# Optimization experiments

Hardware: AMD Instinct MI355X
Metric: run time of the kernel (lower is better)

## Reference

```python
import jax, jax.numpy as jnp
import numpy as np
from jax.ops import segment_sum


def gcn_conv(x, edge_index, W, b):
    """PyG GCNConv: add self-loops, symmetric D^-1/2 (A+I) D^-1/2 normalization,
    then aggregate normalized messages at target nodes. edge_weight=None -> ones."""
    N = x.shape[0]
    loops = jnp.arange(N, dtype=edge_index.dtype)
    row = jnp.concatenate([edge_index[0], loops])  # source nodes
    col = jnp.concatenate([edge_index[1], loops])  # target nodes
    w = jnp.ones(row.shape[0], dtype=x.dtype)
    deg = segment_sum(w, col, num_segments=N)
    dinv = jnp.where(deg > 0, jax.lax.rsqrt(deg), 0.0)
    norm = dinv[row] * dinv[col]                    # [E+N]
    xw = x @ W                                      # dense transform [N, out]
    msg = xw[row] * norm[:, None]                   # gather + scale [E+N, out]
    out = segment_sum(msg, col, num_segments=N)     # scatter-add at targets
    return out + b


def setup_inputs() -> dict:
    key = jax.random.key(0)
    k1, k2, k3, k4 = jax.random.split(key, 4)
    N, E, nhid, nfeat = 50000, 800000, 256, 128
    x = jax.random.normal(k1, (N, nhid), dtype=jnp.float32)
    edge_index = jax.random.randint(k2, (2, E), 0, N, dtype=jnp.int64)
    W1 = jax.random.normal(k3, (nhid, nhid), dtype=jnp.float32) * (1.0 / np.sqrt(nhid))
    b1 = jnp.zeros((nhid,), dtype=jnp.float32)
    W2 = jax.random.normal(k4, (nhid, nfeat), dtype=jnp.float32) * (1.0 / np.sqrt(nhid))
    b2 = jnp.zeros((nfeat,), dtype=jnp.float32)
    return {"x": x, "edge_index": edge_index, "W1": W1, "b1": b1, "W2": W2, "b2": b2}


def reference(x, edge_index, W1, b1, W2, b2):
    h = jax.nn.relu(gcn_conv(x, edge_index, W1, b1))
    # dropout is identity in eval mode (deterministic reference)
    return gcn_conv(h, edge_index, W2, b2)
```

## Files before the change

kernel.cpp:

```cpp
#include <hip/hip_runtime.h>
#include <math.h>


typedef _Float16 h8 __attribute__((ext_vector_type(8)));
typedef float    f32x4 __attribute__((ext_vector_type(4)));

#define CAP 64

__global__ void k_init(int* __restrict__ deg, int* __restrict__ govf, int N,
                       const float* __restrict__ W1, const float* __restrict__ W2,
                       _Float16* __restrict__ wt1, _Float16* __restrict__ wt2,
                       int K, int n1, int n2, int zb)
{
    if ((int)blockIdx.x < zb) {
        int i = blockIdx.x * blockDim.x + threadIdx.x;
        if (i < N) deg[i] = 0;
        if (blockIdx.x == 0 && threadIdx.x == 0) *govf = 0;
    } else {
        int i = (blockIdx.x - zb) * blockDim.x + threadIdx.x;
        int c1 = K * n1;
        if (i < c1) {
            int k = i / n1, n = i % n1;
            wt1[(long)n * K + k] = (_Float16)W1[i];
        } else if (i < c1 + K * n2) {
            int j = i - c1;
            int k = j / n2, n = j % n2;
            wt2[(long)n * K + k] = (_Float16)W2[j];
        }
    }
}

template<bool A32>
__device__ __forceinline__ void gemm_body(
    const float* __restrict__ X32, const _Float16* __restrict__ X16,
    const _Float16* __restrict__ Wt, _Float16* __restrict__ Y,
    int M, int K, int NC, int bx, int by)
{
    __shared__ _Float16 As[128][40];
    __shared__ _Float16 Bs[128][40];

    const int bn = bx * 128;
    const int bm = by * 128;
    const int tid = threadIdx.x;
    const int w = tid >> 6, l = tid & 63;
    const int wm = (w >> 1) * 64, wn = (w & 1) * 64;
    const int lr = l & 15, lg = l >> 4;

    const int arow = tid >> 2, acol = (tid & 3) * 8;
    const int xrow = tid >> 1, xcol = (tid & 1) * 16;

    f32x4 acc[4][4];
    #pragma unroll
    for (int i = 0; i < 4; i++)
        #pragma unroll
        for (int j = 0; j < 4; j++)
            acc[i][j] = (f32x4){0.f, 0.f, 0.f, 0.f};

    float4 pf0, pf1, pf2, pf3;
    h8 pa0, pa1;
    h8 pb0, pb1;

    auto loadA = [&](int k0) {
        if (A32) {
            int gm0 = bm + arow;      if (gm0 >= M) gm0 = M - 1;
            int gm1 = bm + 64 + arow; if (gm1 >= M) gm1 = M - 1;
            pf0 = *reinterpret_cast<const float4*>(&X32[(long)gm0 * K + k0 + acol]);
            pf1 = *reinterpret_cast<const float4*>(&X32[(long)gm0 * K + k0 + acol + 4]);
            pf2 = *reinterpret_cast<const float4*>(&X32[(long)gm1 * K + k0 + acol]);
            pf3 = *reinterpret_cast<const float4*>(&X32[(long)gm1 * K + k0 + acol + 4]);
        } else {
            int gm = bm + xrow; if (gm >= M) gm = M - 1;
            pa0 = *reinterpret_cast<const h8*>(&X16[(long)gm * K + k0 + xcol]);
            pa1 = *reinterpret_cast<const h8*>(&X16[(long)gm * K + k0 + xcol + 8]);
        }
    };
    auto loadB = [&](int k0) {
        pb0 = *reinterpret_cast<const h8*>(&Wt[(long)(bn + xrow) * K + k0 + xcol]);
        pb1 = *reinterpret_cast<const h8*>(&Wt[(long)(bn + xrow) * K + k0 + xcol + 8]);
    };

    loadA(0); loadB(0);
    for (int k0 = 0; k0 < K; k0 += 32) {
        if (A32) {
            h8 h0, h1;
            h0[0] = (_Float16)pf0.x; h0[1] = (_Float16)pf0.y;
            h0[2] = (_Float16)pf0.z; h0[3] = (_Float16)pf0.w;
            h0[4] = (_Float16)pf1.x; h0[5] = (_Float16)pf1.y;
            h0[6] = (_Float16)pf1.z; h0[7] = (_Float16)pf1.w;
            h1[0] = (_Float16)pf2.x; h1[1] = (_Float16)pf2.y;
            h1[2] = (_Float16)pf2.z; h1[3] = (_Float16)pf2.w;
            h1[4] = (_Float16)pf3.x; h1[5] = (_Float16)pf3.y;
            h1[6] = (_Float16)pf3.z; h1[7] = (_Float16)pf3.w;
            *reinterpret_cast<h8*>(&As[arow][acol]) = h0;
            *reinterpret_cast<h8*>(&As[64 + arow][acol]) = h1;
        } else {
            *reinterpret_cast<h8*>(&As[xrow][xcol]) = pa0;
            *reinterpret_cast<h8*>(&As[xrow][xcol + 8]) = pa1;
        }
        *reinterpret_cast<h8*>(&Bs[xrow][xcol]) = pb0;
        *reinterpret_cast<h8*>(&Bs[xrow][xcol + 8]) = pb1;
        __syncthreads();

        if (k0 + 32 < K) { loadA(k0 + 32); loadB(k0 + 32); }

        h8 a[4], b[4];
        #pragma unroll
        for (int i = 0; i < 4; i++)
            a[i] = *reinterpret_cast<const h8*>(&As[wm + i * 16 + lr][lg * 8]);
        #pragma unroll
        for (int j = 0; j < 4; j++)
            b[j] = *reinterpret_cast<const h8*>(&Bs[wn + j * 16 + lr][lg * 8]);
        #pragma unroll
        for (int i = 0; i < 4; i++)
            #pragma unroll
            for (int j = 0; j < 4; j++)
                acc[i][j] = __builtin_amdgcn_mfma_f32_16x16x32_f16(
                    a[i], b[j], acc[i][j], 0, 0, 0);
        __syncthreads();
    }

    #pragma unroll
    for (int i = 0; i < 4; i++) {
        #pragma unroll
        for (int r = 0; r < 4; r++) {
            int gm = bm + wm + i * 16 + lg * 4 + r;
            if (gm < M) {
                #pragma unroll
                for (int j = 0; j < 4; j++)
                    Y[(long)gm * NC + bn + wn + j * 16 + lr] =
                        (_Float16)acc[i][j][r];
            }
        }
    }
}

__global__ __launch_bounds__(256) void k_count_gemm(
    const int* __restrict__ col, int E, int* __restrict__ deg, int* __restrict__ rank,
    int ncb,
    const float* __restrict__ X32, const _Float16* __restrict__ Wt,
    _Float16* __restrict__ Y, int M, int K, int NC, int gx)
{
    if ((int)blockIdx.x < ncb) {
        int i = blockIdx.x * blockDim.x + threadIdx.x;
        int s = ncb * blockDim.x;
        for (int e = i; e < E; e += s) rank[e] = atomicAdd(&deg[col[e]], 1);
        return;
    }
    int gb = blockIdx.x - ncb;
    gemm_body<true>(X32, nullptr, Wt, Y, M, K, NC, gb % gx, gb / gx);
}

__global__ __launch_bounds__(256) void k_fill_dinv(
    const int* __restrict__ row, const int* __restrict__ col,
    const int* __restrict__ rank, int E,
    const int* __restrict__ deg, float* __restrict__ dinv, int N,
    int* __restrict__ srcidx, int2* __restrict__ ovf, int* __restrict__ govf,
    int zb)
{
    if ((int)blockIdx.x < zb) {
        int i = blockIdx.x * blockDim.x + threadIdx.x;
        if (i < N) dinv[i] = rsqrtf(1.f + (float)deg[i]);
        return;
    }
    int g = (blockIdx.x - zb) * blockDim.x + threadIdx.x;
    int nthreads = (gridDim.x - zb) * blockDim.x;
    if ((E & 3) == 0) {
        int G4 = E >> 2;
        for (int q = g; q < G4; q += nthreads) {
            int e = q << 2;
            int4 c4 = *reinterpret_cast<const int4*>(&col[e]);
            int4 r4 = *reinterpret_cast<const int4*>(&row[e]);
            int4 k4 = *reinterpret_cast<const int4*>(&rank[e]);
            if (k4.x < CAP) srcidx[c4.x * CAP + k4.x] = r4.x;
            else { int o = atomicAdd(govf, 1); ovf[o] = make_int2(r4.x, c4.x); }
            if (k4.y < CAP) srcidx[c4.y * CAP + k4.y] = r4.y;
            else { int o = atomicAdd(govf, 1); ovf[o] = make_int2(r4.y, c4.y); }
            if (k4.z < CAP) srcidx[c4.z * CAP + k4.z] = r4.z;
            else { int o = atomicAdd(govf, 1); ovf[o] = make_int2(r4.z, c4.z); }
            if (k4.w < CAP) srcidx[c4.w * CAP + k4.w] = r4.w;
            else { int o = atomicAdd(govf, 1); ovf[o] = make_int2(r4.w, c4.w); }
        }
    } else {
        for (int e = g; e < E; e += nthreads) {
            int c = col[e], r = row[e], k = rank[e];
            if (k < CAP) srcidx[c * CAP + k] = r;
            else { int o = atomicAdd(govf, 1); ovf[o] = make_int2(r, c); }
        }
    }
}

__global__ __launch_bounds__(256) void k_gemm16(
    const _Float16* __restrict__ X16, const _Float16* __restrict__ Wt,
    _Float16* __restrict__ Y, int M, int K, int NC)
{
    gemm_body<false>(nullptr, X16, Wt, Y, M, K, NC, blockIdx.x, blockIdx.y);
}

template<int LPR, bool F16OUT, bool RELU>
__global__ __launch_bounds__(256) void k_agg(
    const int* __restrict__ deg, const float* __restrict__ dinv,
    const int* __restrict__ srcidx,
    const int2* __restrict__ ovf, const int* __restrict__ govf,
    const _Float16* __restrict__ Y, const float* __restrict__ bias,
    int N, int FT, int fo,
    float* __restrict__ out32, _Float16* __restrict__ out16)
{
    const int G = 64 / LPR;
    int node = blockIdx.x * 4 + (threadIdx.x >> 6);
    if (node >= N) return;
    int lane = threadIdx.x & 63;
    int sub = lane / LPR;
    int fl  = lane % LPR;
    const int fcol = fo + fl * 8;

    float dc = dinv[node];
    int cnt = min(deg[node], CAP);
    const int beg = node * CAP;

    float acc[8];
    if (sub == 0) {
        h8 v = *reinterpret_cast<const h8*>(&Y[(long)node * FT + fcol]);
        #pragma unroll
        for (int j = 0; j < 8; j++) acc[j] = dc * (float)v[j];
    } else {
        #pragma unroll
        for (int j = 0; j < 8; j++) acc[j] = 0.f;
    }

    int i = sub;
    int full = cnt / (4 * G);
    for (int t = 0; t < full; t++) {
        int r0 = srcidx[beg + i];
        int r1 = srcidx[beg + i + G];
        int r2 = srcidx[beg + i + 2 * G];
        int r3 = srcidx[beg + i + 3 * G];
        float d0 = dinv[r0], d1 = dinv[r1], d2 = dinv[r2], d3 = dinv[r3];
        h8 v0 = *reinterpret_cast<const h8*>(&Y[(long)r0 * FT + fcol]);
        h8 v1 = *reinterpret_cast<const h8*>(&Y[(long)r1 * FT + fcol]);
        h8 v2 = *reinterpret_cast<const h8*>(&Y[(long)r2 * FT + fcol]);
        h8 v3 = *reinterpret_cast<const h8*>(&Y[(long)r3 * FT + fcol]);
        #pragma unroll
        for (int j = 0; j < 8; j++)
            acc[j] += (d0 * (float)v0[j] + d1 * (float)v1[j]) +
                      (d2 * (float)v2[j] + d3 * (float)v3[j]);
        i += 4 * G;
    }
    for (; i < cnt; i += G) {
        int r = srcidx[beg + i];
        float d = dinv[r];
        h8 v = *reinterpret_cast<const h8*>(&Y[(long)r * FT + fcol]);
        #pragma unroll
        for (int j = 0; j < 8; j++) acc[j] += d * (float)v[j];
    }
    {
        int no = *govf;
        for (int t = sub; t < no; t += G) {
            int2 pr = ovf[t];
            if (pr.y == node) {
                float d = dinv[pr.x];
                h8 v = *reinterpret_cast<const h8*>(&Y[(long)pr.x * FT + fcol]);
                #pragma unroll
                for (int j = 0; j < 8; j++) acc[j] += d * (float)v[j];
            }
        }
    }

    #pragma unroll
    for (int m = LPR; m < 64; m <<= 1)
        #pragma unroll
        for (int j = 0; j < 8; j++)
            acc[j] += __shfl_xor(acc[j], m, 64);

    const float4* b4 = reinterpret_cast<const float4*>(&bias[fcol]);
    float4 blo = b4[0], bhi = b4[1];
    float r8[8];
    r8[0] = fmaf(dc, acc[0], blo.x); r8[1] = fmaf(dc, acc[1], blo.y);
    r8[2] = fmaf(dc, acc[2], blo.z); r8[3] = fmaf(dc, acc[3], blo.w);
    r8[4] = fmaf(dc, acc[4], bhi.x); r8[5] = fmaf(dc, acc[5], bhi.y);
    r8[6] = fmaf(dc, acc[6], bhi.z); r8[7] = fmaf(dc, acc[7], bhi.w);
    if (RELU) {
        #pragma unroll
        for (int j = 0; j < 8; j++) r8[j] = fmaxf(r8[j], 0.f);
    }

    long base = (long)node * FT + fcol;
    if (F16OUT) {
        if (sub == 0) {
            h8 o;
            #pragma unroll
            for (int j = 0; j < 8; j++) o[j] = (_Float16)r8[j];
            *reinterpret_cast<h8*>(&out16[base]) = o;
        }
    } else {
        if (sub == 0) {
            *reinterpret_cast<float4*>(&out32[base]) =
                make_float4(r8[0], r8[1], r8[2], r8[3]);
        } else if (sub == 1) {
            *reinterpret_cast<float4*>(&out32[base + 4]) =
                make_float4(r8[4], r8[5], r8[6], r8[7]);
        }
    }
}

extern "C" void kernel_launch(void* const* d_in, const int* in_sizes, int n_in,
                              void* d_out, int out_size, void* d_ws, size_t ws_size,
                              hipStream_t stream)
{
    const float* x   = (const float*)d_in[0];
    const int*   ei  = (const int*)d_in[1];
    const float* W1  = (const float*)d_in[2];
    const float* b1  = (const float*)d_in[3];
    const float* W2  = (const float*)d_in[4];
    const float* b2  = (const float*)d_in[5];

    const int nhid  = in_sizes[3];
    const int nfeat = in_sizes[5];
    const int N     = in_sizes[0] / nhid;
    const int E     = in_sizes[1] / 2;

    const int* row = ei;
    const int* col = ei + E;

    size_t cur = 0;
    auto alloc = [&](size_t bytes) {
        void* p = (char*)d_ws + cur;
        cur += (bytes + 255) & ~(size_t)255;
        return p;
    };
    float*     dinv   = (float*)alloc((size_t)N * 4);
    int*       deg_i  = (int*)alloc((size_t)N * 4);
    int*       rank   = (int*)alloc((size_t)E * 4);
    int*       srcidx = (int*)alloc((size_t)N * CAP * 4);
    int2*      ovf    = (int2*)alloc((size_t)E * 8);
    int*       govf   = (int*)alloc(256);
    _Float16*  wt1    = (_Float16*)alloc((size_t)nhid * nhid * 2);
    _Float16*  wt2    = (_Float16*)alloc((size_t)nhid * nfeat * 2);
    _Float16*  y16    = (_Float16*)alloc((size_t)N * nhid * 2);
    _Float16*  h16    = (_Float16*)alloc((size_t)N * nhid * 2);
    _Float16*  y2     = (_Float16*)alloc((size_t)N * nfeat * 2);
    float*     out    = (float*)d_out;
    (void)ws_size; (void)n_in; (void)out_size;

    const int T = 256;
    const int zb = (N + T - 1) / T;

    {
        int pb = (nhid * (nhid + nfeat) + T - 1) / T;
        k_init<<<zb + pb, T, 0, stream>>>(deg_i, govf, N, W1, W2, wt1, wt2,
                                          nhid, nhid, nfeat, zb);
    }

    {
        const int ncb = 256;
        int gx = nhid / 128;
        int gy = (N + 127) / 128;
        k_count_gemm<<<ncb + gx * gy, T, 0, stream>>>(
            col, E, deg_i, rank, ncb, x, wt1, y16, N, nhid, nhid, gx);
    }

    k_fill_dinv<<<zb + 1024, T, 0, stream>>>(
        row, col, rank, E, deg_i, dinv, N, srcidx, ovf, govf, zb);

    k_agg<16, true, true><<<(N + 3) / 4, T, 0, stream>>>(
        deg_i, dinv, srcidx, ovf, govf, y16, b1, N, nhid, 0, nullptr, h16);
    k_agg<16, true, true><<<(N + 3) / 4, T, 0, stream>>>(
        deg_i, dinv, srcidx, ovf, govf, y16, b1, N, nhid, 128, nullptr, h16);

    {
        dim3 grid(nfeat / 128, (N + 127) / 128);
        k_gemm16<<<grid, T, 0, stream>>>(h16, wt2, y2, N, nhid, nfeat);
    }
    k_agg<16, false, false><<<(N + 3) / 4, T, 0, stream>>>(
        deg_i, dinv, srcidx, ovf, govf, y2, b2, N, nfeat, 0, out, nullptr);
}
```

Baseline: 180.5 us.

## Split first GEMM column tiles across count and fill kernels for overlap

The first-layer GEMM tiles are now split in half by output column block: one half runs alongside the degree-count atomics, the other half alongside the dinv and bucket-fill work in the following kernel. The count grid also grows from 256 to 512 blocks. The aim is to balance each launch so the memory-bound edge work hides behind compute-bound GEMM blocks, rather than putting all GEMM work into the first launch. The risk is that the GEMM halves now contend with the different edge phases for bandwidth and CUs.

```diff
diff --git a/kernel.cpp b/kernel.cpp
--- a/kernel.cpp
+++ b/kernel.cpp
@@ -138,7 +138,7 @@
     const int* __restrict__ col, int E, int* __restrict__ deg, int* __restrict__ rank,
     int ncb,
     const float* __restrict__ X32, const _Float16* __restrict__ Wt,
-    _Float16* __restrict__ Y, int M, int K, int NC, int gx)
+    _Float16* __restrict__ Y, int M, int K, int NC, int gxA, int bx0)
 {
     if ((int)blockIdx.x < ncb) {
         int i = blockIdx.x * blockDim.x + threadIdx.x;
@@ -147,46 +147,53 @@
         return;
     }
     int gb = blockIdx.x - ncb;
-    gemm_body<true>(X32, nullptr, Wt, Y, M, K, NC, gb % gx, gb / gx);
-}
-
-__global__ __launch_bounds__(256) void k_fill_dinv(
+    gemm_body<true>(X32, nullptr, Wt, Y, M, K, NC, bx0 + gb % gxA, gb / gxA);
+}
+
+__global__ __launch_bounds__(256) void k_fill_gemm(
     const int* __restrict__ row, const int* __restrict__ col,
     const int* __restrict__ rank, int E,
     const int* __restrict__ deg, float* __restrict__ dinv, int N,
     int* __restrict__ srcidx, int2* __restrict__ ovf, int* __restrict__ govf,
-    int zb)
+    int zb, int nfb,
+    const float* __restrict__ X32, const _Float16* __restrict__ Wt,
+    _Float16* __restrict__ Y, int M, int K, int NC, int gxB, int bx0)
 {
     if ((int)blockIdx.x < zb) {
         int i = blockIdx.x * blockDim.x + threadIdx.x;
         if (i < N) dinv[i] = rsqrtf(1.f + (float)deg[i]);
         return;
     }
-    int g = (blockIdx.x - zb) * blockDim.x + threadIdx.x;
-    int nthreads = (gridDim.x - zb) * blockDim.x;
-    if ((E & 3) == 0) {
-        int G4 = E >> 2;
-        for (int q = g; q < G4; q += nthreads) {
-            int e = q << 2;
-            int4 c4 = *reinterpret_cast<const int4*>(&col[e]);
-            int4 r4 = *reinterpret_cast<const int4*>(&row[e]);
-            int4 k4 = *reinterpret_cast<const int4*>(&rank[e]);
-            if (k4.x < CAP) srcidx[c4.x * CAP + k4.x] = r4.x;
-            else { int o = atomicAdd(govf, 1); ovf[o] = make_int2(r4.x, c4.x); }
-            if (k4.y < CAP) srcidx[c4.y * CAP + k4.y] = r4.y;
-            else { int o = atomicAdd(govf, 1); ovf[o] = make_int2(r4.y, c4.y); }
-            if (k4.z < CAP) srcidx[c4.z * CAP + k4.z] = r4.z;
-            else { int o = atomicAdd(govf, 1); ovf[o] = make_int2(r4.z, c4.z); }
-            if (k4.w < CAP) srcidx[c4.w * CAP + k4.w] = r4.w;
-            else { int o = atomicAdd(govf, 1); ovf[o] = make_int2(r4.w, c4.w); }
-        }
-    } else {
-        for (int e = g; e < E; e += nthreads) {
-            int c = col[e], r = row[e], k = rank[e];
-            if (k < CAP) srcidx[c * CAP + k] = r;
-            else { int o = atomicAdd(govf, 1); ovf[o] = make_int2(r, c); }
-        }
-    }
+    if ((int)blockIdx.x < zb + nfb) {
+        int g = (blockIdx.x - zb) * blockDim.x + threadIdx.x;
+        int nthreads = nfb * blockDim.x;
+        if ((E & 3) == 0) {
+            int G4 = E >> 2;
+            for (int q = g; q < G4; q += nthreads) {
+                int e = q << 2;
+                int4 c4 = *reinterpret_cast<const int4*>(&col[e]);
+                int4 r4 = *reinterpret_cast<const int4*>(&row[e]);
+                int4 k4 = *reinterpret_cast<const int4*>(&rank[e]);
+                if (k4.x < CAP) srcidx[c4.x * CAP + k4.x] = r4.x;
+                else { int o = atomicAdd(govf, 1); ovf[o] = make_int2(r4.x, c4.x); }
+                if (k4.y < CAP) srcidx[c4.y * CAP + k4.y] = r4.y;
+                else { int o = atomicAdd(govf, 1); ovf[o] = make_int2(r4.y, c4.y); }
+                if (k4.z < CAP) srcidx[c4.z * CAP + k4.z] = r4.z;
+                else { int o = atomicAdd(govf, 1); ovf[o] = make_int2(r4.z, c4.z); }
+                if (k4.w < CAP) srcidx[c4.w * CAP + k4.w] = r4.w;
+                else { int o = atomicAdd(govf, 1); ovf[o] = make_int2(r4.w, c4.w); }
+            }
+        } else {
+            for (int e = g; e < E; e += nthreads) {
+                int c = col[e], r = row[e], k = rank[e];
+                if (k < CAP) srcidx[c * CAP + k] = r;
+                else { int o = atomicAdd(govf, 1); ovf[o] = make_int2(r, c); }
+            }
+        }
+        return;
+    }
+    int gb = blockIdx.x - zb - nfb;
+    gemm_body<true>(X32, nullptr, Wt, Y, M, K, NC, bx0 + gb % gxB, gb / gxB);
 }
 
 __global__ __launch_bounds__(256) void k_gemm16(
@@ -343,6 +350,10 @@
 
     const int T = 256;
     const int zb = (N + T - 1) / T;
+    const int gx = nhid / 128;
+    const int gy = (N + 127) / 128;
+    const int gxA = (gx + 1) / 2;
+    const int gxB = gx - gxA;
 
     {
         int pb = (nhid * (nhid + nfeat) + T - 1) / T;
@@ -351,15 +362,17 @@
     }
 
     {
-        const int ncb = 256;
-        int gx = nhid / 128;
-        int gy = (N + 127) / 128;
-        k_count_gemm<<<ncb + gx * gy, T, 0, stream>>>(
-            col, E, deg_i, rank, ncb, x, wt1, y16, N, nhid, nhid, gx);
-    }
-
-    k_fill_dinv<<<zb + 1024, T, 0, stream>>>(
-        row, col, rank, E, deg_i, dinv, N, srcidx, ovf, govf, zb);
+        const int ncb = 512;
+        k_count_gemm<<<ncb + gxA * gy, T, 0, stream>>>(
+            col, E, deg_i, rank, ncb, x, wt1, y16, N, nhid, nhid, gxA, 0);
+    }
+
+    {
+        const int nfb = 1024;
+        k_fill_gemm<<<zb + nfb + gxB * gy, T, 0, stream>>>(
+            row, col, rank, E, deg_i, dinv, N, srcidx, ovf, govf, zb, nfb,
+            x, wt1, y16, N, nhid, nhid, gxB, gxA);
+    }
 
     k_agg<16, true, true><<<(N + 3) / 4, T, 0, stream>>>(
         deg_i, dinv, srcidx, ovf, govf, y16, b1, N, nhid, 0, nullptr, h16);
```

Measured after the change: 195.3 us. +8.2%, slower.

## Reschedule kernels: memset init, fuse weight prep with count, GEMM with fill

Applied to the files above, without the earlier changes.

Replaces the init kernel with a hipMemsetAsync over the degree counter and overflow counter, which are now allocated next to each other. The fp16 weight transpose moves into the degree-count kernel, which also gets more counting blocks. The first GEMM now runs alongside the dinv/srcidx fill instead of alongside the count. The two feature-half layer-1 aggregation launches merge into one launch that picks the feature offset from the block index. This cuts launch count and rebalances which independent work overlaps, at the cost of a memset node and changed dependencies: the GEMM now waits for the count and weight prep.

```diff
diff --git a/kernel.cpp b/kernel.cpp
--- a/kernel.cpp
+++ b/kernel.cpp
@@ -6,29 +6,6 @@
 typedef float    f32x4 __attribute__((ext_vector_type(4)));
 
 #define CAP 64
-
-__global__ void k_init(int* __restrict__ deg, int* __restrict__ govf, int N,
-                       const float* __restrict__ W1, const float* __restrict__ W2,
-                       _Float16* __restrict__ wt1, _Float16* __restrict__ wt2,
-                       int K, int n1, int n2, int zb)
-{
-    if ((int)blockIdx.x < zb) {
-        int i = blockIdx.x * blockDim.x + threadIdx.x;
-        if (i < N) deg[i] = 0;
-        if (blockIdx.x == 0 && threadIdx.x == 0) *govf = 0;
-    } else {
-        int i = (blockIdx.x - zb) * blockDim.x + threadIdx.x;
-        int c1 = K * n1;
-        if (i < c1) {
-            int k = i / n1, n = i % n1;
-            wt1[(long)n * K + k] = (_Float16)W1[i];
-        } else if (i < c1 + K * n2) {
-            int j = i - c1;
-            int k = j / n2, n = j % n2;
-            wt2[(long)n * K + k] = (_Float16)W2[j];
-        }
-    }
-}
 
 template<bool A32>
 __device__ __forceinline__ void gemm_body(
@@ -134,11 +111,12 @@
     }
 }
 
-__global__ __launch_bounds__(256) void k_count_gemm(
+__global__ __launch_bounds__(256) void k_count_prep(
     const int* __restrict__ col, int E, int* __restrict__ deg, int* __restrict__ rank,
     int ncb,
-    const float* __restrict__ X32, const _Float16* __restrict__ Wt,
-    _Float16* __restrict__ Y, int M, int K, int NC, int gx)
+    const float* __restrict__ W1, const float* __restrict__ W2,
+    _Float16* __restrict__ wt1, _Float16* __restrict__ wt2,
+    int K, int n1, int n2)
 {
     if ((int)blockIdx.x < ncb) {
         int i = blockIdx.x * blockDim.x + threadIdx.x;
@@ -146,24 +124,39 @@
         for (int e = i; e < E; e += s) rank[e] = atomicAdd(&deg[col[e]], 1);
         return;
     }
-    int gb = blockIdx.x - ncb;
-    gemm_body<true>(X32, nullptr, Wt, Y, M, K, NC, gb % gx, gb / gx);
-}
-
-__global__ __launch_bounds__(256) void k_fill_dinv(
+    int i = (blockIdx.x - ncb) * blockDim.x + threadIdx.x;
+    int c1 = K * n1;
+    if (i < c1) {
+        int k = i / n1, n = i % n1;
+        wt1[(long)n * K + k] = (_Float16)W1[i];
+    } else if (i < c1 + K * n2) {
+        int j = i - c1;
+        int k = j / n2, n = j % n2;
+        wt2[(long)n * K + k] = (_Float16)W2[j];
+    }
+}
+
+__global__ __launch_bounds__(256) void k_gemm_fill(
+    const float* __restrict__ X32, const _Float16* __restrict__ Wt,
+    _Float16* __restrict__ Y, int M, int K, int NC, int ngb, int gx,
     const int* __restrict__ row, const int* __restrict__ col,
     const int* __restrict__ rank, int E,
     const int* __restrict__ deg, float* __restrict__ dinv, int N,
     int* __restrict__ srcidx, int2* __restrict__ ovf, int* __restrict__ govf,
     int zb)
 {
-    if ((int)blockIdx.x < zb) {
-        int i = blockIdx.x * blockDim.x + threadIdx.x;
+    if ((int)blockIdx.x < ngb) {
+        int gb = blockIdx.x;
+        gemm_body<true>(X32, nullptr, Wt, Y, M, K, NC, gb % gx, gb / gx);
+        return;
+    }
+    if ((int)blockIdx.x < ngb + zb) {
+        int i = (blockIdx.x - ngb) * blockDim.x + threadIdx.x;
         if (i < N) dinv[i] = rsqrtf(1.f + (float)deg[i]);
         return;
     }
-    int g = (blockIdx.x - zb) * blockDim.x + threadIdx.x;
-    int nthreads = (gridDim.x - zb) * blockDim.x;
+    int g = (blockIdx.x - ngb - zb) * blockDim.x + threadIdx.x;
+    int nthreads = (gridDim.x - ngb - zb) * blockDim.x;
     if ((E & 3) == 0) {
         int G4 = E >> 2;
         for (int q = g; q < G4; q += nthreads) {
@@ -202,16 +195,18 @@
     const int* __restrict__ srcidx,
     const int2* __restrict__ ovf, const int* __restrict__ govf,
     const _Float16* __restrict__ Y, const float* __restrict__ bias,
-    int N, int FT, int fo,
+    int N, int FT, int nblk,
     float* __restrict__ out32, _Float16* __restrict__ out16)
 {
     const int G = 64 / LPR;
-    int node = blockIdx.x * 4 + (threadIdx.x >> 6);
+    int pass = blockIdx.x / nblk;
+    int bid  = blockIdx.x - pass * nblk;
+    int node = bid * 4 + (threadIdx.x >> 6);
     if (node >= N) return;
     int lane = threadIdx.x & 63;
     int sub = lane / LPR;
     int fl  = lane % LPR;
-    const int fcol = fo + fl * 8;
+    const int fcol = pass * 128 + fl * 8;
 
     float dc = dinv[node];
     int cnt = min(deg[node], CAP);
@@ -327,12 +322,12 @@
         cur += (bytes + 255) & ~(size_t)255;
         return p;
     };
+    int*       deg_i  = (int*)alloc((size_t)N * 4);
+    int*       govf   = (int*)alloc(256);
     float*     dinv   = (float*)alloc((size_t)N * 4);
-    int*       deg_i  = (int*)alloc((size_t)N * 4);
     int*       rank   = (int*)alloc((size_t)E * 4);
     int*       srcidx = (int*)alloc((size_t)N * CAP * 4);
     int2*      ovf    = (int2*)alloc((size_t)E * 8);
-    int*       govf   = (int*)alloc(256);
     _Float16*  wt1    = (_Float16*)alloc((size_t)nhid * nhid * 2);
     _Float16*  wt2    = (_Float16*)alloc((size_t)nhid * nfeat * 2);
     _Float16*  y16    = (_Float16*)alloc((size_t)N * nhid * 2);
@@ -343,33 +338,39 @@
 
     const int T = 256;
     const int zb = (N + T - 1) / T;
-
-    {
+    const int gx = nhid / 128;
+    const int gy = (N + 127) / 128;
+
+    size_t degpad = (((size_t)N * 4) + 255) & ~(size_t)255;
+    hipMemsetAsync(deg_i, 0, degpad + 256, stream);
+
+    {
+        const int ncb = 1024;
         int pb = (nhid * (nhid + nfeat) + T - 1) / T;
-        k_init<<<zb + pb, T, 0, stream>>>(deg_i, govf, N, W1, W2, wt1, wt2,
-                                          nhid, nhid, nfeat, zb);
-    }
-
-    {
-        const int ncb = 256;
-        int gx = nhid / 128;
-        int gy = (N + 127) / 128;
-        k_count_gemm<<<ncb + gx * gy, T, 0, stream>>>(
-            col, E, deg_i, rank, ncb, x, wt1, y16, N, nhid, nhid, gx);
-    }
-
-    k_fill_dinv<<<zb + 1024, T, 0, stream>>>(
-        row, col, rank, E, deg_i, dinv, N, srcidx, ovf, govf, zb);
-
-    k_agg<16, true, true><<<(N + 3) / 4, T, 0, stream>>>(
-        deg_i, dinv, srcidx, ovf, govf, y16, b1, N, nhid, 0, nullptr, h16);
-    k_agg<16, true, true><<<(N + 3) / 4, T, 0, stream>>>(
-        deg_i, dinv, srcidx, ovf, govf, y16, b1, N, nhid, 128, nullptr, h16);
+        k_count_prep<<<ncb + pb, T, 0, stream>>>(
+            col, E, deg_i, rank, ncb, W1, W2, wt1, wt2, nhid, nhid, nfeat);
+    }
+
+    {
+        int ngb = gx * gy;
+        k_gemm_fill<<<ngb + zb + 1024, T, 0, stream>>>(
+            x, wt1, y16, N, nhid, nhid, ngb, gx,
+            row, col, rank, E, deg_i, dinv, N, srcidx, ovf, govf, zb);
+    }
+
+    {
+        int nblk = (N + 3) / 4;
+        k_agg<16, true, true><<<2 * nblk, T, 0, stream>>>(
+            deg_i, dinv, srcidx, ovf, govf, y16, b1, N, nhid, nblk, nullptr, h16);
+    }
 
     {
         dim3 grid(nfeat / 128, (N + 127) / 128);
         k_gemm16<<<grid, T, 0, stream>>>(h16, wt2, y2, N, nhid, nfeat);
     }
-    k_agg<16, false, false><<<(N + 3) / 4, T, 0, stream>>>(
-        deg_i, dinv, srcidx, ovf, govf, y2, b2, N, nfeat, 0, out, nullptr);
-}
+    {
+        int nblk = (N + 3) / 4;
+        k_agg<16, false, false><<<nblk, T, 0, stream>>>(
+            deg_i, dinv, srcidx, ovf, govf, y2, b2, N, nfeat, nblk, out, nullptr);
+    }
+}
```

Measured after the change: 187.0 us. 1.04x slower.
